# Kernel tuning notes

Hardware: AMD Instinct MI355X
Metric: run time of the kernel (lower is better)

## Reference

```python
import jax, jax.numpy as jnp
import numpy as np

EXCHANGE_RATIO = 0.5


def setup_inputs() -> dict:
    key = jax.random.key(0)
    k1, k2, k3, k4 = jax.random.split(key, 4)
    B, C, L = 8, 512, 4096
    x1 = jax.random.normal(k1, (B, C, L), dtype=jnp.float32)
    x2 = jax.random.normal(k2, (B, C, L), dtype=jnp.float32)
    bn1 = jax.random.normal(k3, (C,), dtype=jnp.float32)
    bn2 = jax.random.normal(k4, (C,), dtype=jnp.float32)
    return {"x1": x1, "x2": x2, "bn1": bn1, "bn2": bn2}


def _nontop_indices(bn, topk):
    # channels NOT in topk of |bn|, in ascending index order (matches torch
    # boolean-mask indexing semantics)
    a = jnp.abs(bn)
    C = bn.shape[0]
    _, idx = jax.lax.top_k(a, topk)
    mask = jnp.zeros((C,), dtype=bool).at[idx].set(True)
    # stable argsort of bool puts False (non-top) first, in ascending index order
    nontop = jnp.argsort(mask, stable=True)[: C - topk]
    return nontop


def reference(x1, x2, bn1, bn2):
    C = bn1.shape[0]
    topk = int(C * (1.0 - EXCHANGE_RATIO))  # static: 256
    nontop1 = _nontop_indices(bn1, topk)
    nontop2 = _nontop_indices(bn2, topk)
    # y1 keeps x1's top channels, takes x2's non-top channels (order-aligned)
    y1 = x1.at[:, nontop1, :].set(x2[:, nontop2, :])
    # y2 keeps x2's top channels, takes x1's non-top channels
    y2 = x2.at[:, nontop2, :].set(x1[:, nontop1, :])
    return (y1, y2)
```

## Files before the change

kernel.cpp:

```cpp
#include <hip/hip_runtime.h>
#include <math.h>

#define C_CH   512
#define TOPK   256
#define B_N    8
#define L_LEN  4096
#define L4     (L_LEN / 4)
#define ROWS   (B_N * C_CH)

__global__ __launch_bounds__(C_CH) void build_maps(
        const float* __restrict__ bn1,
        const float* __restrict__ bn2,
        int* __restrict__ map1,
        int* __restrict__ map2) {
    __shared__ float2 a12[C_CH];
    __shared__ int nt1[C_CH - TOPK], nt2[C_CH - TOPK];
    __shared__ int wsum1[8], wsum2[8];
    const int t = threadIdx.x;
    const float v1 = fabsf(bn1[t]);
    const float v2 = fabsf(bn2[t]);
    a12[t] = make_float2(v1, v2);
    __syncthreads();

    int r1 = 0, r2 = 0;
#pragma unroll 8
    for (int j = 0; j < C_CH; ++j) {
        const float2 bj = a12[j];
        r1 += (bj.x > v1) || (bj.x == v1 && j < t);
        r2 += (bj.y > v2) || (bj.y == v2 && j < t);
    }
    const bool non1 = (r1 >= TOPK);
    const bool non2 = (r2 >= TOPK);

    const unsigned long long m1 = __ballot(non1);
    const unsigned long long m2 = __ballot(non2);
    const int lane = t & 63, w = t >> 6;
    const unsigned long long below = (1ULL << lane) - 1ULL;
    const int lp1 = __popcll(m1 & below);
    const int lp2 = __popcll(m2 & below);
    if (lane == 0) { wsum1[w] = __popcll(m1); wsum2[w] = __popcll(m2); }
    __syncthreads();
    int base1 = 0, base2 = 0;
#pragma unroll
    for (int i = 0; i < 8; ++i) {
        base1 += (i < w) ? wsum1[i] : 0;
        base2 += (i < w) ? wsum2[i] : 0;
    }
    const int p1 = base1 + lp1;
    const int p2 = base2 + lp2;
    if (non1) nt1[p1] = t;
    if (non2) nt2[p2] = t;
    __syncthreads();

    map1[t] = non1 ? (C_CH + nt2[p1]) : t;
    map2[t] = non2 ? (C_CH + nt1[p2]) : t;
}

__global__ __launch_bounds__(256) void exchange_copy(
        const float4* __restrict__ x1,
        const float4* __restrict__ x2,
        const int* __restrict__ map1,
        const int* __restrict__ map2,
        float4* __restrict__ y1,
        float4* __restrict__ y2) {
    const int row = blockIdx.x;
    const int c = row & (C_CH - 1);
    const int b = row >> 9;

    const int m1 = map1[c];
    const int m2 = map2[c];
    const float4* __restrict__ s1 = (m1 < C_CH) ? x1 : x2;
    const float4* __restrict__ s2 = (m2 < C_CH) ? x2 : x1;
    const size_t src1 = (size_t)((b << 9) | (m1 & (C_CH - 1))) << 10;
    const size_t src2 = (size_t)((b << 9) | (m2 & (C_CH - 1))) << 10;
    const size_t dst  = (size_t)row << 10;

    const float4* __restrict__ p1 = s1 + src1;
    const float4* __restrict__ p2 = s2 + src2;
    float4* __restrict__ q1 = y1 + dst;
    float4* __restrict__ q2 = y2 + dst;

    const int t = threadIdx.x;
    float4 r[4], s[4];
#pragma unroll
    for (int k = 0; k < 4; ++k) r[k] = p1[t + 256 * k];
#pragma unroll
    for (int k = 0; k < 4; ++k) s[k] = p2[t + 256 * k];
#pragma unroll
    for (int k = 0; k < 4; ++k) q1[t + 256 * k] = r[k];
#pragma unroll
    for (int k = 0; k < 4; ++k) q2[t + 256 * k] = s[k];
}

extern "C" void kernel_launch(void* const* d_in, const int* in_sizes, int n_in,
                              void* d_out, int out_size, void* d_ws, size_t ws_size,
                              hipStream_t stream) {
    const float* x1  = (const float*)d_in[0];
    const float* x2  = (const float*)d_in[1];
    const float* bn1 = (const float*)d_in[2];
    const float* bn2 = (const float*)d_in[3];

    float* y1 = (float*)d_out;
    float* y2 = (float*)d_out + (B_N * C_CH * L_LEN);

    int* map1 = (int*)d_ws;
    int* map2 = map1 + C_CH;

    build_maps<<<1, C_CH, 0, stream>>>(bn1, bn2, map1, map2);

    exchange_copy<<<ROWS, 256, 0, stream>>>(
        (const float4*)x1, (const float4*)x2, map1, map2,
        (float4*)y1, (float4*)y2);
}
```

Baseline: 267.8 us.

## Replace fused gather copy with bulk memcpy plus swapped-channel fixup kernel

The per-row gather kernel is replaced by two full device-to-device hipMemcpyAsync copies of x1 and x2 into the outputs. A smaller kernel then overwrites only the exchanged non-top channels. The map-building kernel now writes the non-top index lists straight to global memory. The aim is to use the runtime's copy path for the bulk traffic, but half the channels are written twice, which adds memory traffic, and the work is split across extra launches.

```diff
diff --git a/kernel.cpp b/kernel.cpp
--- a/kernel.cpp
+++ b/kernel.cpp
@@ -3,18 +3,19 @@
 
 #define C_CH   512
 #define TOPK   256
+#define NPAIR  (C_CH - TOPK)
 #define B_N    8
 #define L_LEN  4096
 #define L4     (L_LEN / 4)
-#define ROWS   (B_N * C_CH)
+#define TENSOR_BYTES ((size_t)B_N * C_CH * L_LEN * 4)
+
 
 __global__ __launch_bounds__(C_CH) void build_maps(
         const float* __restrict__ bn1,
         const float* __restrict__ bn2,
-        int* __restrict__ map1,
-        int* __restrict__ map2) {
+        int* __restrict__ nt1g,
+        int* __restrict__ nt2g) {
     __shared__ float2 a12[C_CH];
-    __shared__ int nt1[C_CH - TOPK], nt2[C_CH - TOPK];
     __shared__ int wsum1[8], wsum2[8];
     const int t = threadIdx.x;
     const float v1 = fabsf(bn1[t]);
@@ -46,50 +47,38 @@
         base1 += (i < w) ? wsum1[i] : 0;
         base2 += (i < w) ? wsum2[i] : 0;
     }
-    const int p1 = base1 + lp1;
-    const int p2 = base2 + lp2;
-    if (non1) nt1[p1] = t;
-    if (non2) nt2[p2] = t;
-    __syncthreads();
-
-    map1[t] = non1 ? (C_CH + nt2[p1]) : t;
-    map2[t] = non2 ? (C_CH + nt1[p2]) : t;
+    if (non1) nt1g[base1 + lp1] = t;
+    if (non2) nt2g[base2 + lp2] = t;
 }
 
-__global__ __launch_bounds__(256) void exchange_copy(
+__global__ __launch_bounds__(256) void exchange_fix(
         const float4* __restrict__ x1,
         const float4* __restrict__ x2,
-        const int* __restrict__ map1,
-        const int* __restrict__ map2,
+        const int* __restrict__ nt1,
+        const int* __restrict__ nt2,
         float4* __restrict__ y1,
         float4* __restrict__ y2) {
-    const int row = blockIdx.x;
-    const int c = row & (C_CH - 1);
-    const int b = row >> 9;
+    const int blk = blockIdx.x;
+    const int p = blk & (NPAIR - 1);
+    const int b = blk >> 8;
+    const int c1 = nt1[p];
+    const int c2 = nt2[p];
 
-    const int m1 = map1[c];
-    const int m2 = map2[c];
-    const float4* __restrict__ s1 = (m1 < C_CH) ? x1 : x2;
-    const float4* __restrict__ s2 = (m2 < C_CH) ? x2 : x1;
-    const size_t src1 = (size_t)((b << 9) | (m1 & (C_CH - 1))) << 10;
-    const size_t src2 = (size_t)((b << 9) | (m2 & (C_CH - 1))) << 10;
-    const size_t dst  = (size_t)row << 10;
-
-    const float4* __restrict__ p1 = s1 + src1;
-    const float4* __restrict__ p2 = s2 + src2;
-    float4* __restrict__ q1 = y1 + dst;
-    float4* __restrict__ q2 = y2 + dst;
+    const float4* __restrict__ s1 = x2 + ((size_t)((b << 9) | c2) << 10);
+    float4* __restrict__       d1 = y1 + ((size_t)((b << 9) | c1) << 10);
+    const float4* __restrict__ s2 = x1 + ((size_t)((b << 9) | c1) << 10);
+    float4* __restrict__       d2 = y2 + ((size_t)((b << 9) | c2) << 10);
 
     const int t = threadIdx.x;
-    float4 r[4], s[4];
+    float4 ra[4], rb[4];
 #pragma unroll
-    for (int k = 0; k < 4; ++k) r[k] = p1[t + 256 * k];
+    for (int k = 0; k < 4; ++k) ra[k] = s1[t + 256 * k];
 #pragma unroll
-    for (int k = 0; k < 4; ++k) s[k] = p2[t + 256 * k];
+    for (int k = 0; k < 4; ++k) rb[k] = s2[t + 256 * k];
 #pragma unroll
-    for (int k = 0; k < 4; ++k) q1[t + 256 * k] = r[k];
+    for (int k = 0; k < 4; ++k) d1[t + 256 * k] = ra[k];
 #pragma unroll
-    for (int k = 0; k < 4; ++k) q2[t + 256 * k] = s[k];
+    for (int k = 0; k < 4; ++k) d2[t + 256 * k] = rb[k];
 }
 
 extern "C" void kernel_launch(void* const* d_in, const int* in_sizes, int n_in,
@@ -103,12 +92,15 @@
     float* y1 = (float*)d_out;
     float* y2 = (float*)d_out + (B_N * C_CH * L_LEN);
 
-    int* map1 = (int*)d_ws;
-    int* map2 = map1 + C_CH;
+    int* nt1 = (int*)d_ws;
+    int* nt2 = nt1 + NPAIR;
 
-    build_maps<<<1, C_CH, 0, stream>>>(bn1, bn2, map1, map2);
+    build_maps<<<1, C_CH, 0, stream>>>(bn1, bn2, nt1, nt2);
 
-    exchange_copy<<<ROWS, 256, 0, stream>>>(
-        (const float4*)x1, (const float4*)x2, map1, map2,
+    hipMemcpyAsync(y1, x1, TENSOR_BYTES, hipMemcpyDeviceToDevice, stream);
+    hipMemcpyAsync(y2, x2, TENSOR_BYTES, hipMemcpyDeviceToDevice, stream);
+
+    exchange_fix<<<B_N * NPAIR, 256, 0, stream>>>(
+        (const float4*)x1, (const float4*)x2, nt1, nt2,
         (float4*)y1, (float4*)y2);
 }
```

Result: slower. 284.1 us (+6.1%).
